# Optimization experiments

Measured on AMD Instinct MI355X. Metric: run time of the kernel, lower is better.

## Reference

```python
import jax, jax.numpy as jnp
import numpy as np

NUM_USERS = 100000
NUM_ITEMS = 200000
N = NUM_USERS + NUM_ITEMS
D = 64
NNZ = 5_000_000
B = 16384
N_LAYERS = 3


def setup_inputs() -> dict:
    key = jax.random.key(0)
    ks = jax.random.split(key, 7)
    users = jax.random.randint(ks[0], (B,), 0, NUM_USERS, dtype=jnp.int32)
    items = jax.random.randint(ks[1], (B,), 0, NUM_ITEMS, dtype=jnp.int32)
    edge_row = jax.random.randint(ks[2], (NNZ,), 0, N, dtype=jnp.int32)
    edge_col = jax.random.randint(ks[3], (NNZ,), 0, N, dtype=jnp.int32)
    # mimic D^-1/2 A D^-1/2 normalization scale (~1/avg_degree)
    edge_vals = jax.random.uniform(ks[4], (NNZ,), dtype=jnp.float32) * 0.06
    user_emb = jax.random.normal(ks[5], (NUM_USERS, D), dtype=jnp.float32) * 0.1
    item_emb = jax.random.normal(ks[6], (NUM_ITEMS, D), dtype=jnp.float32) * 0.1
    return {
        "users": users, "items": items,
        "edge_row": edge_row, "edge_col": edge_col, "edge_vals": edge_vals,
        "user_emb": user_emb, "item_emb": item_emb,
        "n_layers": N_LAYERS,
    }


def _spmm(edge_row, edge_col, edge_vals, x):
    # sparse [N,N] @ dense [N,D] via gather + segment_sum
    msg = x[edge_col] * edge_vals[:, None]  # [nnz, D]
    return jax.ops.segment_sum(msg, edge_row, num_segments=N)


def reference(users, items, edge_row, edge_col, edge_vals, user_emb, item_emb, n_layers):
    # LightGCN.computer(): propagate + mean over layers (running-sum form)
    all_emb = jnp.concatenate([user_emb, item_emb], axis=0)  # [N, D]
    acc = all_emb
    for _ in range(n_layers):
        all_emb = _spmm(edge_row, edge_col, edge_vals, all_emb)
        acc = acc + all_emb
    light_out = acc / (n_layers + 1)
    all_users = light_out[:NUM_USERS]
    all_items = light_out[NUM_USERS:]
    # forward(users, items): elementwise dot product
    users_emb = all_users[users]
    items_emb = all_items[items]
    gamma = jnp.sum(users_emb * items_emb, axis=1)  # [B]
    return gamma
```

## Files before the change

kernel.cpp:

```cpp
#include <hip/hip_runtime.h>
#include <hip/hip_fp16.h>
#include <hip/hip_fp8.h>

namespace {

constexpr int kUsers = 100000;
constexpr int kItems = 200000;
constexpr int kN     = kUsers + kItems;
constexpr int kD     = 64;
constexpr int kNNZ   = 5000000;
constexpr int kB     = 16384;
constexpr int kRowsPerBkt = 2048;
constexpr int kNBKT  = (kN + kRowsPerBkt - 1) / kRowsPerBkt;
constexpr int kSEPB  = 4096;
constexpr int kCap   = 40960;
constexpr int kMaxSub = 2 * kB;

typedef int   v2i __attribute__((ext_vector_type(2)));
typedef float v4f __attribute__((ext_vector_type(4)));

#if defined(__has_builtin)
#if __has_builtin(__builtin_amdgcn_cvt_pk_f32_fp8) && __has_builtin(__builtin_amdgcn_cvt_f32_fp8)
#define NATIVE_FP8 1
#endif
#endif
#ifndef NATIVE_FP8
#define NATIVE_FP8 0
#endif

constexpr float kValScale = NATIVE_FP8 ? 1.0f : 256.0f;

__device__ inline void dec8(v2i h, float* f) {
#if NATIVE_FP8
  auto a0 = __builtin_amdgcn_cvt_pk_f32_fp8(h.x, false);
  auto a1 = __builtin_amdgcn_cvt_pk_f32_fp8(h.x, true);
  auto a2 = __builtin_amdgcn_cvt_pk_f32_fp8(h.y, false);
  auto a3 = __builtin_amdgcn_cvt_pk_f32_fp8(h.y, true);
  f[0] = a0[0]; f[1] = a0[1]; f[2] = a1[0]; f[3] = a1[1];
  f[4] = a2[0]; f[5] = a2[1]; f[6] = a3[0]; f[7] = a3[1];
#else
  unsigned int ws[2] = {(unsigned int)h.x, (unsigned int)h.y};
#pragma unroll
  for (int q = 0; q < 2; ++q) {
    unsigned int w = ws[q];
    unsigned int a = ((w & 0x007f007fu) << 7) | ((w & 0x00800080u) << 8);
    unsigned int b = (((w >> 8) & 0x007f007fu) << 7) | (((w >> 8) & 0x00800080u) << 8);
    float2 e = __half22float2(*reinterpret_cast<const __half2*>(&a));
    float2 o = __half22float2(*reinterpret_cast<const __half2*>(&b));
    f[4 * q + 0] = e.x; f[4 * q + 1] = o.x; f[4 * q + 2] = e.y; f[4 * q + 3] = o.y;
  }
#endif
}

__device__ inline float dec1(unsigned char b) {
#if NATIVE_FP8
  return __builtin_amdgcn_cvt_f32_fp8((int)b, 0) * 0.015625f;
#else
  unsigned int hb = ((b & 0x7fu) << 7) | ((b & 0x80u) << 8);
  return __half2float(__ushort_as_half((unsigned short)hb)) * 4.0f;
#endif
}

__device__ inline unsigned char enc(float f) { __hip_fp8_e4m3 q(f); return q.__x; }

__device__ inline float vdec(int w) {
  return __half2float(__ushort_as_half((unsigned short)((w >> 17) & 0x7FFC))) * kValScale;
}

__global__ void zero3(int* __restrict__ gpos, int* __restrict__ mark,
                      int* __restrict__ dh, int* __restrict__ scnt) {
  int i = blockIdx.x * blockDim.x + threadIdx.x;
  if (i < kN) mark[i] = 0;
  if (i < kNBKT + 1) gpos[i] = 0;
  if (i < 64) dh[i] = 0;
  if (i == 0) scnt[0] = 0;
}

__global__ void bucket_scatter(const int* __restrict__ row, const int* __restrict__ col,
                               const float* __restrict__ val, int* __restrict__ gpos,
                               int* __restrict__ tmp4, unsigned short* __restrict__ tmpr) {
  __shared__ int hcnt[4][kNBKT];
  __shared__ int lofs[kNBKT];
  __shared__ int hbase[kNBKT];
  __shared__ int lds[256];
  __shared__ int sp[kSEPB];
  __shared__ unsigned short sr[kSEPB];
  __shared__ unsigned short sb[kSEPB];
  int t = threadIdx.x;
  int wv = t >> 6;
  long base = (long)blockIdx.x * kSEPB;
  int valid = (int)min((long)kSEPB, (long)kNNZ - base);
  for (int i = t; i < kNBKT; i += 256) {
    hcnt[0][i] = 0; hcnt[1][i] = 0; hcnt[2][i] = 0; hcnt[3][i] = 0;
  }
  __syncthreads();
  int py[16], bk[16], rl[16], rk[16];
  bool ok[16];
#pragma unroll
  for (int j = 0; j < 16; ++j) {
    long i = base + j * 256 + t;
    ok[j] = (i < kNNZ);
    if (ok[j]) {
      int r = __builtin_nontemporal_load(row + i);
      int c = __builtin_nontemporal_load(col + i);
      float v = __builtin_nontemporal_load(val + i);
      bk[j] = r >> 11;
      rl[j] = r & 2047;
      unsigned short hb = __half_as_ushort(__float2half_rn(v));
      int v13 = ((int)hb + 2) >> 2;
      py[j] = c | (v13 << 19);
      rk[j] = atomicAdd(&hcnt[wv][bk[j]], 1);
    }
  }
  __syncthreads();
  int own = 0;
  if (t < kNBKT) {
    int c0 = hcnt[0][t], c1 = hcnt[1][t], c2 = hcnt[2][t], c3 = hcnt[3][t];
    hcnt[0][t] = 0; hcnt[1][t] = c0; hcnt[2][t] = c0 + c1; hcnt[3][t] = c0 + c1 + c2;
    own = c0 + c1 + c2 + c3;
  }
  lds[t] = own;
  __syncthreads();
  for (int o = 1; o < 256; o <<= 1) {
    int x = (t >= o) ? lds[t - o] : 0;
    __syncthreads();
    if (t >= o) lds[t] += x;
    __syncthreads();
  }
  if (t < kNBKT) {
    lofs[t] = lds[t] - own;
    hbase[t] = t * kCap + atomicAdd(&gpos[t], own);
  }
  __syncthreads();
#pragma unroll
  for (int j = 0; j < 16; ++j) {
    if (ok[j]) {
      int pos = lofs[bk[j]] + hcnt[wv][bk[j]] + rk[j];
      sp[pos] = py[j];
      sr[pos] = (unsigned short)rl[j];
      sb[pos] = (unsigned short)bk[j];
    }
  }
  __syncthreads();
#pragma unroll
  for (int j = 0; j < 16; ++j) {
    int pos = t + j * 256;
    if (pos < valid) {
      int b = sb[pos];
      int w = hbase[b] + (pos - lofs[b]);
      tmp4[w] = sp[pos];
      tmpr[w] = sr[pos];
    }
  }
}

__global__ __launch_bounds__(1024) void build_csr(
    const int* __restrict__ gpos, const int* __restrict__ tmp4,
    const unsigned short* __restrict__ tmpr, int* __restrict__ rowptr,
    int* __restrict__ edges) {
  __shared__ int h[kRowsPerBkt];
  __shared__ int lsum[256];
  __shared__ int gscan[256];
  int b = blockIdx.x, t = threadIdx.x;
  if (t < 256) gscan[t] = (t < kNBKT) ? gpos[t] : 0;
  for (int i = t; i < kRowsPerBkt; i += 1024) h[i] = 0;
  __syncthreads();
  for (int o = 1; o < 256; o <<= 1) {
    int v = 0;
    if (t < 256 && t >= o) v = gscan[t - o];
    __syncthreads();
    if (t < 256 && t >= o) gscan[t] += v;
    __syncthreads();
  }
  int bucket_base = (b == 0) ? 0 : gscan[b - 1];
  int s = b * kCap;
  int e = s + gpos[b];
  for (int j = s + t; j < e; j += 1024) atomicAdd(&h[tmpr[j]], 1);
  __syncthreads();
  int cnt[8], pref[8];
  if (t < 256) {
    int acc = 0;
#pragma unroll
    for (int k = 0; k < 8; ++k) {
      cnt[k] = h[t * 8 + k];
      pref[k] = acc;
      acc += cnt[k];
    }
    lsum[t] = acc;
  }
  __syncthreads();
  for (int o = 1; o < 256; o <<= 1) {
    int v = 0;
    if (t < 256 && t >= o) v = lsum[t - o];
    __syncthreads();
    if (t < 256 && t >= o) lsum[t] += v;
    __syncthreads();
  }
  if (t < 256) {
    int ex = (t == 0) ? 0 : lsum[t - 1];
#pragma unroll
    for (int k = 0; k < 8; ++k) {
      int g = bucket_base + ex + pref[k];
      int r = b * kRowsPerBkt + t * 8 + k;
      if (r < kN) rowptr[r] = g;
      h[t * 8 + k] = g;
    }
  }
  if (b == kNBKT - 1 && t == 0) rowptr[kN] = kNNZ;
  __syncthreads();
  for (int j = s + t; j < e; j += 1024) {
    int pay = tmp4[j];
    int rl = tmpr[j];
    int dst = atomicAdd(&h[rl], 1);
    edges[dst] = pay;
  }
}

__global__ void mark_rows(const int* __restrict__ users, const int* __restrict__ items,
                          int* __restrict__ mark) {
  int i = blockIdx.x * blockDim.x + threadIdx.x;
  if (i >= kB) return;
  mark[users[i]] = 1;
  mark[kUsers + items[i]] = 1;
}

__global__ void sub_hist(const int* __restrict__ rowptr, const int* __restrict__ mark,
                         int* __restrict__ dh) {
  __shared__ int h[64];
  int t = threadIdx.x;
  if (t < 64) h[t] = 0;
  __syncthreads();
  int i = blockIdx.x * 256 + t;
  if (i < kN && mark[i]) {
    int d = min(rowptr[i + 1] - rowptr[i], 63);
    atomicAdd(&h[d], 1);
  }
  __syncthreads();
  if (t < 64 && h[t]) atomicAdd(&dh[t], h[t]);
}

__global__ void deg_scan(int* __restrict__ dh, int* __restrict__ scnt) {
  int t = threadIdx.x;
  int v = dh[t];
  int x = v;
  for (int o = 1; o < 64; o <<= 1) {
    int y = __shfl_up(x, o, 64);
    if (t >= o) x += y;
  }
  if (t == 63) *scnt = x;
  dh[t] = x - v;
}

__global__ void sub_place(const int* __restrict__ rowptr, const int* __restrict__ mark,
                          int* __restrict__ dh, int* __restrict__ list) {
  __shared__ int h[64], base[64];
  int t = threadIdx.x;
  if (t < 64) h[t] = 0;
  __syncthreads();
  int i = blockIdx.x * 256 + t;
  int d = 0, lr = 0;
  bool okv = (i < kN) && mark[i];
  if (okv) {
    d = min(rowptr[i + 1] - rowptr[i], 63);
    lr = atomicAdd(&h[d], 1);
  }
  __syncthreads();
  if (t < 64) base[t] = h[t] ? atomicAdd(&dh[t], h[t]) : 0;
  __syncthreads();
  if (okv) list[base[d] + lr] = i;
}

__global__ void mark_cols(const int* __restrict__ list, const int* __restrict__ cnt,
                          const int* __restrict__ rowptr, const int* __restrict__ edges,
                          int* __restrict__ mark) {
  int p = blockIdx.x * blockDim.x + threadIdx.x;
  if (p >= *cnt) return;
  int r = list[p];
  int s = rowptr[r], e = rowptr[r + 1];
  for (int j = s; j < e; ++j) mark[edges[j] & 0x7FFFF] = 1;
}

__global__ void to_fp8(const float* __restrict__ ue, const float* __restrict__ ie,
                       unsigned char* __restrict__ xq) {
  int t = blockIdx.x * blockDim.x + threadIdx.x;
  if (t >= kN * kD / 8) return;
  int row = t >> 3;
  int seg = t & 7;
  const float* src = (row < kUsers) ? (ue + (size_t)row * kD + seg * 8)
                                    : (ie + (size_t)(row - kUsers) * kD + seg * 8);
  v4f a = __builtin_nontemporal_load((const v4f*)src);
  v4f b = __builtin_nontemporal_load((const v4f*)src + 1);
  float f[8] = {a.x, a.y, a.z, a.w, b.x, b.y, b.z, b.w};
  unsigned int w0 = 0, w1 = 0;
#pragma unroll
  for (int k = 0; k < 4; ++k) w0 |= (unsigned int)enc(f[k] * 64.f) << (8 * k);
#pragma unroll
  for (int k = 0; k < 4; ++k) w1 |= (unsigned int)enc(f[4 + k] * 64.f) << (8 * k);
  v2i o; o.x = (int)w0; o.y = (int)w1;
  ((v2i*)xq)[t] = o;
}

template <int MODE>
__global__ __launch_bounds__(256, 8) void spmm(
    const int* __restrict__ rowptr, const int* __restrict__ edges,
    const unsigned char* __restrict__ x, unsigned char* __restrict__ yq,
    const int* __restrict__ aux, const int* __restrict__ cnt) {
  int t = threadIdx.x;
  int l = t & 7;
  int wid = (blockIdx.x * 256 + t) >> 6;
  int g = (t >> 3) & 7;
  int p = wid * 8 + g;
  int r = -1;
  bool live = false;
  if (MODE == 2) {
    int n = *cnt;
    if (p < n) { r = aux[p]; live = true; }
  } else {
    if (p < kN) { r = p; live = (MODE == 0) || (aux[r] != 0); }
  }
  int s = 0, e = 0;
  if (live) { s = rowptr[r]; e = rowptr[r + 1]; }
  int mx = e - s;
#pragma unroll
  for (int m = 8; m <= 32; m <<= 1) mx = max(mx, __shfl_xor(mx, m, 64));
  float acc[8];
#pragma unroll
  for (int k = 0; k < 8; ++k) acc[k] = 0.f;
  int last = max(e - 1, 0);
  int j = s;
  int E0 = edges[min(j, last)];
  int E1 = edges[min(j + 1, last)];
  int E2 = edges[min(j + 2, last)];
  int E3 = edges[min(j + 3, last)];
  for (int it = 0; it < mx; it += 4) {
    float v0 = (j     < e) ? vdec(E0) : 0.f;
    float v1 = (j + 1 < e) ? vdec(E1) : 0.f;
    float v2 = (j + 2 < e) ? vdec(E2) : 0.f;
    float v3 = (j + 3 < e) ? vdec(E3) : 0.f;
    v2i h0 = ((const v2i*)(x + (size_t)(E0 & 0x7FFFF) * kD))[l];
    v2i h1 = ((const v2i*)(x + (size_t)(E1 & 0x7FFFF) * kD))[l];
    v2i h2 = ((const v2i*)(x + (size_t)(E2 & 0x7FFFF) * kD))[l];
    v2i h3 = ((const v2i*)(x + (size_t)(E3 & 0x7FFFF) * kD))[l];
    j += 4;
    E0 = edges[min(j, last)];
    E1 = edges[min(j + 1, last)];
    E2 = edges[min(j + 2, last)];
    E3 = edges[min(j + 3, last)];
    float f[8];
    dec8(h0, f);
#pragma unroll
    for (int k = 0; k < 8; ++k) acc[k] = fmaf(v0, f[k], acc[k]);
    dec8(h1, f);
#pragma unroll
    for (int k = 0; k < 8; ++k) acc[k] = fmaf(v1, f[k], acc[k]);
    dec8(h2, f);
#pragma unroll
    for (int k = 0; k < 8; ++k) acc[k] = fmaf(v2, f[k], acc[k]);
    dec8(h3, f);
#pragma unroll
    for (int k = 0; k < 8; ++k) acc[k] = fmaf(v3, f[k], acc[k]);
  }
  if (live) {
    unsigned int w0 = 0, w1 = 0;
#pragma unroll
    for (int k = 0; k < 4; ++k) w0 |= (unsigned int)enc(acc[k]) << (8 * k);
#pragma unroll
    for (int k = 0; k < 4; ++k) w1 |= (unsigned int)enc(acc[4 + k]) << (8 * k);
    v2i o; o.x = (int)w0; o.y = (int)w1;
    ((v2i*)yq)[(size_t)r * 8 + l] = o;
  }
}

__global__ void acc_add_init(const int* __restrict__ users, const int* __restrict__ items,
                             const float* __restrict__ uemb, const float* __restrict__ iemb,
                             const unsigned char* __restrict__ xq, float* __restrict__ uacc,
                             float* __restrict__ iacc) {
  int tid = blockIdx.x * blockDim.x + threadIdx.x;
  if (tid >= kB * kD) return;
  int b = tid >> 6, d = tid & 63;
  int u = users[b], iw = items[b];
  uacc[tid] = uemb[(size_t)u * kD + d] + dec1(xq[(size_t)u * kD + d]);
  iacc[tid] = iemb[(size_t)iw * kD + d] + dec1(xq[(size_t)(kUsers + iw) * kD + d]);
}

__global__ void acc_add(const int* __restrict__ users, const int* __restrict__ items,
                        const unsigned char* __restrict__ xq, float* __restrict__ uacc,
                        float* __restrict__ iacc) {
  int tid = blockIdx.x * blockDim.x + threadIdx.x;
  if (tid >= kB * kD) return;
  int b = tid >> 6, d = tid & 63;
  uacc[tid] += dec1(xq[(size_t)users[b] * kD + d]);
  iacc[tid] += dec1(xq[(size_t)(kUsers + items[b]) * kD + d]);
}

__global__ void acc_add_fin(const int* __restrict__ users, const int* __restrict__ items,
                            const unsigned char* __restrict__ xq, const float* __restrict__ uacc,
                            const float* __restrict__ iacc, float* __restrict__ out) {
  int tid = blockIdx.x * blockDim.x + threadIdx.x;
  if (tid >= kB * kD) return;
  int b = tid >> 6, d = tid & 63;
  float u = uacc[tid] + dec1(xq[(size_t)users[b] * kD + d]);
  float v = iacc[tid] + dec1(xq[(size_t)(kUsers + items[b]) * kD + d]);
  float p = u * v;
  for (int o = 32; o > 0; o >>= 1) p += __shfl_down(p, o, 64);
  if (d == 0) out[b] = p * 0.0625f;
}

}

extern "C" void kernel_launch(void* const* d_in, const int* in_sizes, int n_in,
                              void* d_out, int out_size, void* d_ws, size_t ws_size,
                              hipStream_t stream) {
  const int*   users = (const int*)d_in[0];
  const int*   items = (const int*)d_in[1];
  const int*   erow  = (const int*)d_in[2];
  const int*   ecol  = (const int*)d_in[3];
  const float* evals = (const float*)d_in[4];
  const float* uemb  = (const float*)d_in[5];
  const float* iemb  = (const float*)d_in[6];
  float* out = (float*)d_out;

  char* ws = (char*)d_ws;
  size_t off = 0;
  auto take = [&](size_t bytes) -> char* {
    char* p = ws + off;
    off = (off + bytes + 255) & ~(size_t)255;
    return p;
  };
  int*    rowptr   = (int*)take((size_t)(kN + 1) * 4);
  int*    gpos     = (int*)take((kNBKT + 1) * 4);
  int*    dh       = (int*)take(256 * 4);
  int*    mark     = (int*)take((size_t)kN * 4);
  int*    list     = (int*)take((size_t)kMaxSub * 4);
  int*    scnt     = (int*)take(256);
  int*    edges    = (int*)take((size_t)kNNZ * 4);
  int*    tmp4     = (int*)take((size_t)kNBKT * kCap * 4);
  unsigned short* tmpr = (unsigned short*)take((size_t)kNBKT * kCap * 2);
  unsigned char* xq0 = (unsigned char*)take((size_t)kN * kD);
  unsigned char* xq1 = (unsigned char*)take((size_t)kN * kD);
  float*  uacc     = (float*)take((size_t)kB * kD * 4);
  float*  iacc     = (float*)take((size_t)kB * kD * 4);
  (void)ws_size; (void)in_sizes; (void)n_in; (void)out_size;

  const int nScatBlocks = (kNNZ + kSEPB - 1) / kSEPB;
  const int nSpmmBlocks = (kN + 31) / 32;
  const int nSubBlocks  = (kMaxSub + 31) / 32;
  const int nRowBlocks  = (kN + 255) / 256;

  zero3<<<nRowBlocks, 256, 0, stream>>>(gpos, mark, dh, scnt);
  bucket_scatter<<<nScatBlocks, 256, 0, stream>>>(erow, ecol, evals, gpos, tmp4, tmpr);
  build_csr<<<kNBKT, 1024, 0, stream>>>(gpos, tmp4, tmpr, rowptr, edges);

  mark_rows<<<(kB + 255) / 256, 256, 0, stream>>>(users, items, mark);
  sub_hist<<<nRowBlocks, 256, 0, stream>>>(rowptr, mark, dh);
  deg_scan<<<1, 64, 0, stream>>>(dh, scnt);
  sub_place<<<nRowBlocks, 256, 0, stream>>>(rowptr, mark, dh, list);
  mark_cols<<<(kMaxSub + 255) / 256, 256, 0, stream>>>(list, scnt, rowptr, edges, mark);

  to_fp8<<<(kN * kD / 8 + 255) / 256, 256, 0, stream>>>(uemb, iemb, xq0);
  spmm<0><<<nSpmmBlocks, 256, 0, stream>>>(rowptr, edges, xq0, xq1, nullptr, nullptr);
  acc_add_init<<<(kB * kD) / 256, 256, 0, stream>>>(users, items, uemb, iemb, xq1, uacc, iacc);
  spmm<1><<<nSpmmBlocks, 256, 0, stream>>>(rowptr, edges, xq1, xq0, mark, nullptr);
  acc_add<<<(kB * kD) / 256, 256, 0, stream>>>(users, items, xq0, uacc, iacc);
  spmm<2><<<nSubBlocks, 256, 0, stream>>>(rowptr, edges, xq0, xq1, list, scnt);
  acc_add_fin<<<(kB * kD) / 256, 256, 0, stream>>>(users, items, xq1, uacc, iacc, out);
}
```

Baseline: 483.0 us.

## Split CSR build per half-bucket, ballot-compact rows, fuse layer accumulation

build_csr now launches two blocks per bucket, each placing edges only for its half of the rows, which doubles parallelism at the cost of both blocks re-reading the bucket and recomputing the histogram. The degree-sorted subset list (hist, scan, place) is replaced by a single wave-ballot compaction kernel, so sub-rows are no longer grouped by degree. The three per-layer accumulate kernels become one finalize kernel that reads three kept fp8 layer buffers, which removes the float accumulator traffic but needs an extra N×D buffer.

```diff
diff --git a/kernel.cpp b/kernel.cpp
--- a/kernel.cpp
+++ b/kernel.cpp
@@ -68,11 +68,10 @@
 }
 
 __global__ void zero3(int* __restrict__ gpos, int* __restrict__ mark,
-                      int* __restrict__ dh, int* __restrict__ scnt) {
+                      int* __restrict__ scnt) {
   int i = blockIdx.x * blockDim.x + threadIdx.x;
   if (i < kN) mark[i] = 0;
   if (i < kNBKT + 1) gpos[i] = 0;
-  if (i < 64) dh[i] = 0;
   if (i == 0) scnt[0] = 0;
 }
 
@@ -161,7 +160,9 @@
   __shared__ int h[kRowsPerBkt];
   __shared__ int lsum[256];
   __shared__ int gscan[256];
-  int b = blockIdx.x, t = threadIdx.x;
+  int b = blockIdx.x >> 1;
+  int half = blockIdx.x & 1;
+  int t = threadIdx.x;
   if (t < 256) gscan[t] = (t < kNBKT) ? gpos[t] : 0;
   for (int i = t; i < kRowsPerBkt; i += 1024) h[i] = 0;
   __syncthreads();
@@ -202,17 +203,19 @@
     for (int k = 0; k < 8; ++k) {
       int g = bucket_base + ex + pref[k];
       int r = b * kRowsPerBkt + t * 8 + k;
-      if (r < kN) rowptr[r] = g;
+      if (half == 0 && r < kN) rowptr[r] = g;
       h[t * 8 + k] = g;
     }
   }
-  if (b == kNBKT - 1 && t == 0) rowptr[kN] = kNNZ;
-  __syncthreads();
+  if (blockIdx.x == 0 && t == 0) rowptr[kN] = kNNZ;
+  __syncthreads();
+  int lo = half << 10, hi = lo + 1024;
   for (int j = s + t; j < e; j += 1024) {
-    int pay = tmp4[j];
     int rl = tmpr[j];
-    int dst = atomicAdd(&h[rl], 1);
-    edges[dst] = pay;
+    if (rl >= lo && rl < hi) {
+      int dst = atomicAdd(&h[rl], 1);
+      edges[dst] = tmp4[j];
+    }
   }
 }
 
@@ -224,50 +227,28 @@
   mark[kUsers + items[i]] = 1;
 }
 
-__global__ void sub_hist(const int* __restrict__ rowptr, const int* __restrict__ mark,
-                         int* __restrict__ dh) {
-  __shared__ int h[64];
+__global__ void compact_rows(const int* __restrict__ mark, int* __restrict__ list,
+                             int* __restrict__ cnt) {
+  __shared__ int wbase[4];
   int t = threadIdx.x;
-  if (t < 64) h[t] = 0;
-  __syncthreads();
   int i = blockIdx.x * 256 + t;
-  if (i < kN && mark[i]) {
-    int d = min(rowptr[i + 1] - rowptr[i], 63);
-    atomicAdd(&h[d], 1);
-  }
-  __syncthreads();
-  if (t < 64 && h[t]) atomicAdd(&dh[t], h[t]);
-}
-
-__global__ void deg_scan(int* __restrict__ dh, int* __restrict__ scnt) {
-  int t = threadIdx.x;
-  int v = dh[t];
-  int x = v;
-  for (int o = 1; o < 64; o <<= 1) {
-    int y = __shfl_up(x, o, 64);
-    if (t >= o) x += y;
-  }
-  if (t == 63) *scnt = x;
-  dh[t] = x - v;
-}
-
-__global__ void sub_place(const int* __restrict__ rowptr, const int* __restrict__ mark,
-                          int* __restrict__ dh, int* __restrict__ list) {
-  __shared__ int h[64], base[64];
-  int t = threadIdx.x;
-  if (t < 64) h[t] = 0;
-  __syncthreads();
-  int i = blockIdx.x * 256 + t;
-  int d = 0, lr = 0;
-  bool okv = (i < kN) && mark[i];
-  if (okv) {
-    d = min(rowptr[i + 1] - rowptr[i], 63);
-    lr = atomicAdd(&h[d], 1);
-  }
-  __syncthreads();
-  if (t < 64) base[t] = h[t] ? atomicAdd(&dh[t], h[t]) : 0;
-  __syncthreads();
-  if (okv) list[base[d] + lr] = i;
+  bool m = (i < kN) && mark[i];
+  unsigned long long bal = __ballot(m);
+  int wv = t >> 6, ln = t & 63;
+  if (ln == 0) wbase[wv] = __popcll(bal);
+  __syncthreads();
+  if (t == 0) {
+    int tot = wbase[0] + wbase[1] + wbase[2] + wbase[3];
+    int base = tot ? atomicAdd(cnt, tot) : 0;
+    int p = base;
+#pragma unroll
+    for (int w = 0; w < 4; ++w) { int c = wbase[w]; wbase[w] = p; p += c; }
+  }
+  __syncthreads();
+  if (m) {
+    int rank = __popcll(bal & ((1ull << ln) - 1));
+    list[wbase[wv] + rank] = i;
+  }
 }
 
 __global__ void mark_cols(const int* __restrict__ list, const int* __restrict__ cnt,
@@ -371,37 +352,19 @@
   }
 }
 
-__global__ void acc_add_init(const int* __restrict__ users, const int* __restrict__ items,
-                             const float* __restrict__ uemb, const float* __restrict__ iemb,
-                             const unsigned char* __restrict__ xq, float* __restrict__ uacc,
-                             float* __restrict__ iacc) {
+__global__ void finalize(const int* __restrict__ users, const int* __restrict__ items,
+                         const float* __restrict__ uemb, const float* __restrict__ iemb,
+                         const unsigned char* __restrict__ l1,
+                         const unsigned char* __restrict__ l2,
+                         const unsigned char* __restrict__ l3, float* __restrict__ out) {
   int tid = blockIdx.x * blockDim.x + threadIdx.x;
   if (tid >= kB * kD) return;
   int b = tid >> 6, d = tid & 63;
-  int u = users[b], iw = items[b];
-  uacc[tid] = uemb[(size_t)u * kD + d] + dec1(xq[(size_t)u * kD + d]);
-  iacc[tid] = iemb[(size_t)iw * kD + d] + dec1(xq[(size_t)(kUsers + iw) * kD + d]);
-}
-
-__global__ void acc_add(const int* __restrict__ users, const int* __restrict__ items,
-                        const unsigned char* __restrict__ xq, float* __restrict__ uacc,
-                        float* __restrict__ iacc) {
-  int tid = blockIdx.x * blockDim.x + threadIdx.x;
-  if (tid >= kB * kD) return;
-  int b = tid >> 6, d = tid & 63;
-  uacc[tid] += dec1(xq[(size_t)users[b] * kD + d]);
-  iacc[tid] += dec1(xq[(size_t)(kUsers + items[b]) * kD + d]);
-}
-
-__global__ void acc_add_fin(const int* __restrict__ users, const int* __restrict__ items,
-                            const unsigned char* __restrict__ xq, const float* __restrict__ uacc,
-                            const float* __restrict__ iacc, float* __restrict__ out) {
-  int tid = blockIdx.x * blockDim.x + threadIdx.x;
-  if (tid >= kB * kD) return;
-  int b = tid >> 6, d = tid & 63;
-  float u = uacc[tid] + dec1(xq[(size_t)users[b] * kD + d]);
-  float v = iacc[tid] + dec1(xq[(size_t)(kUsers + items[b]) * kD + d]);
-  float p = u * v;
+  size_t u = (size_t)users[b] * kD + d;
+  size_t iw = (size_t)(kUsers + items[b]) * kD + d;
+  float us = uemb[(size_t)users[b] * kD + d] + dec1(l1[u]) + dec1(l2[u]) + dec1(l3[u]);
+  float vs = iemb[(size_t)items[b] * kD + d] + dec1(l1[iw]) + dec1(l2[iw]) + dec1(l3[iw]);
+  float p = us * vs;
   for (int o = 32; o > 0; o >>= 1) p += __shfl_down(p, o, 64);
   if (d == 0) out[b] = p * 0.0625f;
 }
@@ -429,7 +392,6 @@
   };
   int*    rowptr   = (int*)take((size_t)(kN + 1) * 4);
   int*    gpos     = (int*)take((kNBKT + 1) * 4);
-  int*    dh       = (int*)take(256 * 4);
   int*    mark     = (int*)take((size_t)kN * 4);
   int*    list     = (int*)take((size_t)kMaxSub * 4);
   int*    scnt     = (int*)take(256);
@@ -438,8 +400,7 @@
   unsigned short* tmpr = (unsigned short*)take((size_t)kNBKT * kCap * 2);
   unsigned char* xq0 = (unsigned char*)take((size_t)kN * kD);
   unsigned char* xq1 = (unsigned char*)take((size_t)kN * kD);
-  float*  uacc     = (float*)take((size_t)kB * kD * 4);
-  float*  iacc     = (float*)take((size_t)kB * kD * 4);
+  unsigned char* xq2 = (unsigned char*)take((size_t)kN * kD);
   (void)ws_size; (void)in_sizes; (void)n_in; (void)out_size;
 
   const int nScatBlocks = (kNNZ + kSEPB - 1) / kSEPB;
@@ -447,21 +408,18 @@
   const int nSubBlocks  = (kMaxSub + 31) / 32;
   const int nRowBlocks  = (kN + 255) / 256;
 
-  zero3<<<nRowBlocks, 256, 0, stream>>>(gpos, mark, dh, scnt);
+  zero3<<<nRowBlocks, 256, 0, stream>>>(gpos, mark, scnt);
   bucket_scatter<<<nScatBlocks, 256, 0, stream>>>(erow, ecol, evals, gpos, tmp4, tmpr);
-  build_csr<<<kNBKT, 1024, 0, stream>>>(gpos, tmp4, tmpr, rowptr, edges);
+  build_csr<<<2 * kNBKT, 1024, 0, stream>>>(gpos, tmp4, tmpr, rowptr, edges);
 
   mark_rows<<<(kB + 255) / 256, 256, 0, stream>>>(users, items, mark);
-  sub_hist<<<nRowBlocks, 256, 0, stream>>>(rowptr, mark, dh);
-  deg_scan<<<1, 64, 0, stream>>>(dh, scnt);
-  sub_place<<<nRowBlocks, 256, 0, stream>>>(rowptr, mark, dh, list);
+  compact_rows<<<nRowBlocks, 256, 0, stream>>>(mark, list, scnt);
   mark_cols<<<(kMaxSub + 255) / 256, 256, 0, stream>>>(list, scnt, rowptr, edges, mark);
 
   to_fp8<<<(kN * kD / 8 + 255) / 256, 256, 0, stream>>>(uemb, iemb, xq0);
   spmm<0><<<nSpmmBlocks, 256, 0, stream>>>(rowptr, edges, xq0, xq1, nullptr, nullptr);
-  acc_add_init<<<(kB * kD) / 256, 256, 0, stream>>>(users, items, uemb, iemb, xq1, uacc, iacc);
-  spmm<1><<<nSpmmBlocks, 256, 0, stream>>>(rowptr, edges, xq1, xq0, mark, nullptr);
-  acc_add<<<(kB * kD) / 256, 256, 0, stream>>>(users, items, xq0, uacc, iacc);
-  spmm<2><<<nSubBlocks, 256, 0, stream>>>(rowptr, edges, xq0, xq1, list, scnt);
-  acc_add_fin<<<(kB * kD) / 256, 256, 0, stream>>>(users, items, xq1, uacc, iacc, out);
-}
+  spmm<1><<<nSpmmBlocks, 256, 0, stream>>>(rowptr, edges, xq1, xq2, mark, nullptr);
+  spmm<2><<<nSubBlocks, 256, 0, stream>>>(rowptr, edges, xq2, xq0, list, scnt);
+  finalize<<<(kB * kD) / 256, 256, 0, stream>>>(users, items, uemb, iemb,
+                                                xq1, xq2, xq0, out);
+}
```

After: 460.7 us. 1.05x faster.
